# Performance work log

Hardware: AMD Instinct MI355X
Metric: run time of the kernel (lower is better)

The kernel has to match this reference:

```python
import jax, jax.numpy as jnp
import numpy as np

GRID_DIMS = (64, 64, 64)
GRID_LOWER = np.array([0.0, 0.0, 0.0], np.float32)
GRID_STEPS = np.array([0.015625, 0.015625, 0.015625], np.float32)
RADIUS = 0.03125
STENCIL = 2  # ceil(radius / step)


def _poly6(d2, h):
    # standard SPH poly6 smoothing kernel: 315/(64 pi h^9) (h^2 - d^2)^3, d <= h
    c = np.float32(315.0 / (64.0 * np.pi * h ** 9))
    return jnp.where(d2 <= h * h, c * (h * h - d2) ** 3, 0.0)


def particles2grid(locs, data, density):
    # locs [B,N,3], data [B,N,C], density [B,N] -> grid [B,X,Y,Z,C]
    B, N, _ = locs.shape
    C = data.shape[-1]
    X, Y, Z = GRID_DIMS
    dims = jnp.array(GRID_DIMS, jnp.int32)
    r = jnp.arange(-STENCIL, STENCIL + 1)
    offs = jnp.stack(jnp.meshgrid(r, r, r, indexing='ij'), -1).reshape(-1, 3)  # [K,3]
    base = jnp.floor((locs - GRID_LOWER) / GRID_STEPS).astype(jnp.int32)        # [B,N,3]
    cells = base[:, :, None, :] + offs                                          # [B,N,K,3]
    centers = GRID_LOWER + (cells.astype(locs.dtype) + 0.5) * GRID_STEPS
    d2 = jnp.sum((centers - locs[:, :, None, :]) ** 2, -1)                      # [B,N,K]
    w = _poly6(d2, RADIUS)
    w = jnp.where(jnp.all((cells >= 0) & (cells < dims), -1), w, 0.0)
    contrib = w[..., None] * (data / density[..., None])[:, :, None, :]         # [B,N,K,C]
    cells = jnp.clip(cells, 0, dims - 1)
    flat = (cells[..., 0] * Y + cells[..., 1]) * Z + cells[..., 2]              # [B,N,K]

    def splat(f, c):
        return jnp.zeros((X * Y * Z, C), data.dtype).at[f.reshape(-1)].add(c.reshape(-1, C))

    return jax.vmap(splat)(flat, contrib).reshape(B, X, Y, Z, C)


def grid2particles(grid, locs):
    # trilinear interpolation of grid [B,X,Y,Z,C] at particle locations [B,N,3]
    B, X, Y, Z, C = grid.shape
    dims = jnp.array([X, Y, Z], jnp.int32)
    pos = (locs - GRID_LOWER) / GRID_STEPS - 0.5                                # cell-center coords
    i0 = jnp.floor(pos).astype(jnp.int32)
    frac = pos - i0.astype(locs.dtype)
    gflat = grid.reshape(B, X * Y * Z, C)
    gather = jax.vmap(lambda g, f: g[f])                                        # [B,N] -> [B,N,C]
    out = jnp.zeros((B, locs.shape[1], C), grid.dtype)
    for dx in (0, 1):
        for dy in (0, 1):
            for dz in (0, 1):
                off = jnp.array([dx, dy, dz], jnp.int32)
                idx = i0 + off
                wd = jnp.where(off == 1, frac, 1.0 - frac)                      # [B,N,3]
                w = wd[..., 0] * wd[..., 1] * wd[..., 2]
                w = jnp.where(jnp.all((idx >= 0) & (idx < dims), -1), w, 0.0)
                idx = jnp.clip(idx, 0, dims - 1)
                flat = (idx[..., 0] * Y + idx[..., 1]) * Z + idx[..., 2]
                out = out + w[..., None] * gather(gflat, flat)
    return out


def conv3d(x, w, b):
    y = jax.lax.conv_general_dilated(x, w, (1, 1, 1), 'SAME',
                                     dimension_numbers=('NCDHW', 'OIDHW', 'NCDHW'))
    return y + b[None, :, None, None, None]


def prelu(x, a):
    return jnp.where(x >= 0, x, a * x)


def setup_inputs() -> dict:
    key = jax.random.key(0)
    ks = jax.random.split(key, 8)
    B, N = 2, 32768
    Cin, K, Cout = 4, 32, 4
    s = lambda fan: np.float32(1.0 / np.sqrt(fan * 27))
    return {
        'locs': jax.random.uniform(ks[0], (B, N, 3), jnp.float32),
        'data': jax.random.normal(ks[1], (B, N, Cin), jnp.float32),
        'density': jax.random.uniform(ks[2], (B, N), jnp.float32, 0.5, 1.5),
        'W0': jax.random.normal(ks[3], (K, Cin, 3, 3, 3), jnp.float32) * s(Cin),
        'b0': jnp.zeros((K,), jnp.float32),
        'W1': jax.random.normal(ks[4], (K, K, 3, 3, 3), jnp.float32) * s(K),
        'b1': jnp.zeros((K,), jnp.float32),
        'W2': jax.random.normal(ks[5], (K, K, 3, 3, 3), jnp.float32) * s(K),
        'b2': jnp.zeros((K,), jnp.float32),
        'W3': jax.random.normal(ks[6], (Cout, K, 3, 3, 3), jnp.float32) * s(K),
        'b3': jnp.zeros((Cout,), jnp.float32),
        'a0': jnp.full((1,), 0.25, jnp.float32),
        'a1': jnp.full((1,), 0.25, jnp.float32),
        'a2': jnp.full((1,), 0.25, jnp.float32),
    }


def reference(locs, data, density, W0, b0, W1, b1, W2, b2, W3, b3, a0, a1, a2):
    grid = particles2grid(locs, data, density)            # [B,X,Y,Z,Cin]
    g = jnp.transpose(grid, (0, 4, 1, 2, 3))              # NCDHW
    g = prelu(conv3d(g, W0, b0), a0)
    g = prelu(conv3d(g, W1, b1), a1)
    g = prelu(conv3d(g, W2, b2), a2)
    g = conv3d(g, W3, b3)
    g = jnp.transpose(g, (0, 2, 3, 4, 1))                 # [B,X,Y,Z,Cout]
    return grid2particles(g, locs)                        # [B,N,Cout]
```

## Files before the change

### kernel.cpp

```cpp
#include <hip/hip_runtime.h>

#define BATCH 2
#define NPART 32768
#define GD 64
#define NVOX (BATCH * GD * GD * GD)

typedef unsigned short ushortT;
typedef __attribute__((ext_vector_type(8))) short short8;
typedef __attribute__((ext_vector_type(16))) float float16;

__device__ __forceinline__ float poly6_c() {
    const double H9 = 1.0 / 35184372088832.0;
    return (float)(315.0 / (64.0 * 3.14159265358979323846 * H9));
}

__device__ __forceinline__ ushortT bf16_rne(float f) {
    unsigned int u = __float_as_uint(f);
    u = (u + 0x7fffu + ((u >> 16) & 1u)) >> 16;
    return (ushortT)u;
}

__device__ __forceinline__ int imax(int a, int b) { return a > b ? a : b; }
__device__ __forceinline__ int imin(int a, int b) { return a < b ? a : b; }

__device__ __forceinline__ void load_lds16(const void* g, void* l) {
    __builtin_amdgcn_global_load_lds(
        (const __attribute__((address_space(1))) void*)g,
        (__attribute__((address_space(3))) void*)l, 16, 0, 0);
}

__global__ __launch_bounds__(256) void prep_kernel(
    int* __restrict__ zp,
    const float* __restrict__ W0, const float* __restrict__ W1,
    const float* __restrict__ W2, const float* __restrict__ W3,
    short* __restrict__ Bp) {
    int bid = blockIdx.x, tid = threadIdx.x;
    if (bid < 513) {
        int t = bid * 256 + tid;
        if (t < 131088) zp[t] = 0;
        return;
    }
    int t = (bid - 513) * 256 + tid;
    if (t >= 176 * 512) return;
    int kt = t >> 9;
    int l = (t >> 3) & 63, j = t & 7;
    int n = l & 31, q = l >> 5;
    float v = 0.f;
    if (kt < 14) {
        int k = kt * 16 + 8 * q + j;
        int tap = k >> 3, ic = k & 7;
        if (tap < 27 && ic < 4) v = W0[(n * 4 + ic) * 27 + tap];
    } else {
        const float* W; int O, s;
        if (kt < 68)       { W = W1; O = 32; s = kt - 14; }
        else if (kt < 122) { W = W2; O = 32; s = kt - 68; }
        else               { W = W3; O = 4;  s = kt - 122; }
        int h = s / 27, ss = s - h * 27;
        int gI = ss / 3, dy = ss - gI * 3;
        int dx = gI / 3, dz = gI - dx * 3;
        int tap = dx * 9 + dy * 3 + dz;
        int ic = h * 16 + q * 8 + j;
        if (n < O) v = W[(n * 32 + ic) * 27 + tap];
    }
    Bp[t] = (short)bf16_rne(v);
}

__global__ __launch_bounds__(256) void bin_count_kernel(
    const float* __restrict__ locs, int* __restrict__ counts) {
    int t = blockIdx.x * blockDim.x + threadIdx.x;
    if (t >= BATCH * NPART) return;
    int b = t >> 15;
    int bx = ((int)floorf(locs[t * 3 + 0] * 64.0f)) >> 1;
    int by = ((int)floorf(locs[t * 3 + 1] * 64.0f)) >> 1;
    int bz = ((int)floorf(locs[t * 3 + 2] * 64.0f)) >> 1;
    atomicAdd(&counts[b * 32768 + ((bx * 32) + by) * 32 + bz], 1);
}

__global__ __launch_bounds__(256) void scanA_kernel(
    const int* __restrict__ counts, int* __restrict__ offsets,
    int* __restrict__ blockSum) {
    __shared__ int sh[256];
    int tid = threadIdx.x, g = blockIdx.x;
    int v = counts[g * 256 + tid];
    sh[tid] = v;
    __syncthreads();
    for (int off = 1; off < 256; off <<= 1) {
        int u = (tid >= off) ? sh[tid - off] : 0;
        __syncthreads();
        sh[tid] += u;
        __syncthreads();
    }
    offsets[g * 256 + tid] = sh[tid] - v;
    if (tid == 255) blockSum[g] = sh[255];
}

__global__ __launch_bounds__(256) void scanB_kernel(
    int* __restrict__ offsets, const int* __restrict__ blockSum) {
    __shared__ int sh[256];
    int tid = threadIdx.x, g = blockIdx.x;
    sh[tid] = (tid < g) ? blockSum[tid] : 0;
    __syncthreads();
    for (int off = 128; off > 0; off >>= 1) {
        if (tid < off) sh[tid] += sh[tid + off];
        __syncthreads();
    }
    offsets[g * 256 + tid] += sh[0];
    if (g == 255 && tid == 255) offsets[65536] = BATCH * NPART;
}

__global__ __launch_bounds__(256) void bin_scatter_kernel(
    const float* __restrict__ locs, const float* __restrict__ data,
    const float* __restrict__ density, const int* __restrict__ offsets,
    int* __restrict__ cursor, float* __restrict__ payload) {
    int t = blockIdx.x * blockDim.x + threadIdx.x;
    if (t >= BATCH * NPART) return;
    int b = t >> 15;
    float px = locs[t * 3 + 0];
    float py = locs[t * 3 + 1];
    float pz = locs[t * 3 + 2];
    int bx = ((int)floorf(px * 64.0f)) >> 1;
    int by = ((int)floorf(py * 64.0f)) >> 1;
    int bz = ((int)floorf(pz * 64.0f)) >> 1;
    int bb = b * 32768 + ((bx * 32) + by) * 32 + bz;
    int slot = atomicAdd(&cursor[bb], 1);
    int idx = offsets[bb] + slot;
    float inv_d = 1.0f / density[t];
    float4 p0 = {px, py, pz, data[t * 4 + 0] * inv_d};
    float4 p1 = {data[t * 4 + 1] * inv_d, data[t * 4 + 2] * inv_d,
                 data[t * 4 + 3] * inv_d, 0.f};
    *(float4*)(payload + idx * 8)     = p0;
    *(float4*)(payload + idx * 8 + 4) = p1;
}

__global__ __launch_bounds__(256) void splat_gather_kernel(
    const float* __restrict__ payload, const int* __restrict__ offsets,
    ushortT* __restrict__ g8) {
    __shared__ float plist[256 * 8];
    __shared__ int segS[36];
    __shared__ int segP[37];
    __shared__ int shTot[1];

    int wg = blockIdx.x;
    int sb = wg & 511, b = wg >> 9;
    int X0 = (sb >> 6) * 8, Y0 = ((sb >> 3) & 7) * 8, Z0 = (sb & 7) * 8;
    int tid = threadIdx.x;

    int bxlo = imax(0, (X0 - 2) >> 1), bxhi = imin(31, (X0 + 9) >> 1);
    int bylo = imax(0, (Y0 - 2) >> 1), byhi = imin(31, (Y0 + 9) >> 1);
    int bzlo = imax(0, (Z0 - 2) >> 1), bzhi = imin(31, (Z0 + 9) >> 1);
    int ny = byhi - bylo + 1;
    int ns = (bxhi - bxlo + 1) * ny;
    if (tid < ns) {
        int bx = bxlo + tid / ny, by = bylo + tid % ny;
        int row = b * 32768 + (bx * 32 + by) * 32;
        int s = offsets[row + bzlo];
        int e = offsets[row + bzhi + 1];
        segS[tid] = s;
        segP[tid] = e - s;
    }
    __syncthreads();
    if (tid == 0) {
        int p = 0;
        for (int k = 0; k < ns; ++k) { int len = segP[k]; segP[k] = p; p += len; }
        segP[ns] = p;
        shTot[0] = p;
    }
    __syncthreads();

    const float step = 0.015625f;
    const float h2 = 0.03125f * 0.03125f;
    const float cc = poly6_c();
    int total = shTot[0];

    int l = tid & 63, w = tid >> 6;
    int cx = X0 + 4 * (w >> 1) + (l >> 4);
    int cy = Y0 + 4 * (w & 1) + ((l >> 2) & 3);
    int cz0 = Z0 + (l & 3);
    float xc  = ((float)cx  + 0.5f) * step;
    float yc  = ((float)cy  + 0.5f) * step;
    float zc0 = ((float)cz0 + 0.5f) * step;
    float zc1 = zc0 + 4.0f * step;

    float a00 = 0.f, a01 = 0.f, a02 = 0.f, a03 = 0.f;
    float a10 = 0.f, a11 = 0.f, a12 = 0.f, a13 = 0.f;

    int nchunks = (total + 255) >> 8;
    for (int ch = 0; ch < nchunks; ++ch) {
        __syncthreads();
        int jj = (ch << 8) + tid;
        if (jj < total) {
            int k = 0;
            while (jj >= segP[k + 1]) ++k;
            int idx = segS[k] + (jj - segP[k]);
            *(float4*)(plist + tid * 8)     = *(const float4*)(payload + idx * 8);
            *(float4*)(plist + tid * 8 + 4) = *(const float4*)(payload + idx * 8 + 4);
        }
        __syncthreads();
        int cnt = imin(256, total - (ch << 8));
        for (int p = 0; p < cnt; ++p) {
            float4 pa = *(const float4*)(plist + p * 8);
            float dx = pa.x - xc, dy = pa.y - yc;
            float dxy2 = fmaf(dy, dy, dx * dx);
            if (!__any(dxy2 <= h2)) continue;
            float4 pv = *(const float4*)(plist + p * 8 + 4);
            float dz0 = pa.z - zc0;
            float d20 = fmaf(dz0, dz0, dxy2);
            float u0 = fmaxf(h2 - d20, 0.f);
            float w0 = (cc * u0) * (u0 * u0);
            a00 = fmaf(w0, pa.w, a00);
            a01 = fmaf(w0, pv.x, a01);
            a02 = fmaf(w0, pv.y, a02);
            a03 = fmaf(w0, pv.z, a03);
            float dz1 = pa.z - zc1;
            float d21 = fmaf(dz1, dz1, dxy2);
            float u1 = fmaxf(h2 - d21, 0.f);
            float w1 = (cc * u1) * (u1 * u1);
            a10 = fmaf(w1, pa.w, a10);
            a11 = fmaf(w1, pv.x, a11);
            a12 = fmaf(w1, pv.y, a12);
            a13 = fmaf(w1, pv.z, a13);
        }
    }

    size_t cellBase = (size_t)(((b * 64 + cx) * 64 + cy) * 64);
    short8 o;
    o[0] = (short)bf16_rne(a00); o[1] = (short)bf16_rne(a01);
    o[2] = (short)bf16_rne(a02); o[3] = (short)bf16_rne(a03);
    o[4] = 0; o[5] = 0; o[6] = 0; o[7] = 0;
    *(short8*)(g8 + (cellBase + cz0) * 8) = o;
    o[0] = (short)bf16_rne(a10); o[1] = (short)bf16_rne(a11);
    o[2] = (short)bf16_rne(a12); o[3] = (short)bf16_rne(a13);
    *(short8*)(g8 + (cellBase + cz0 + 4) * 8) = o;
}

template <int ICG, int KT, bool FINAL>
__global__ __launch_bounds__(256, 4) void mfma_conv_kernel(
    const ushortT* __restrict__ in, const short* __restrict__ Bpack,
    const float* __restrict__ bias, const float* __restrict__ alpha,
    const float* __restrict__ zguard, void* __restrict__ outv) {
    constexpr int CIN = ICG * 8;
    constexpr int NCH = (ICG == 1) ? (36 * 34) : (36 * 2 * 34);
    __shared__ short lds[NCH * 8];
    int wg = ((blockIdx.x & 7) << 7) | (blockIdx.x >> 3);
    int zh = wg & 1, yq = (wg >> 1) & 15, xp = (wg >> 5) & 15, b = wg >> 9;
    int X0 = xp * 4, Y0 = yq * 4, Z0 = zh * 32;
    int tid = threadIdx.x;

    const ushortT* inb = in + (size_t)b * (64 * 64 * 64 * CIN);

    int l = tid & 63, w = tid >> 6;
    int n = l & 31, q = l >> 5;

    float bval = FINAL ? (n < 4 ? bias[n] : 0.f) : bias[n];
    float16 acc0, acc1, acc2, acc3;
#pragma unroll
    for (int r = 0; r < 16; ++r) {
        acc0[r] = bval; acc1[r] = bval; acc2[r] = bval; acc3[r] = bval;
    }

    const short* bp = Bpack + (size_t)l * 8;
    int laneZ = (l & 31) * 8;

    short8 bf[4];
#pragma unroll
    for (int i = 0; i < 4; ++i) bf[i] = *(const short8*)(bp + i * 512);

    if constexpr (ICG == 1) {
#pragma unroll
        for (int it = 0; it < (NCH + 255) / 256; ++it) {
            int ccid = it * 256 + tid;
            if (ccid < NCH) {
                int col = ccid / 34;
                int zi  = ccid - col * 34;
                int gx = X0 + col / 6 - 1;
                int gy = Y0 + col % 6 - 1;
                int gz = Z0 + zi - 1;
                const void* src = (const void*)zguard;
                if ((unsigned)gx < 64u && (unsigned)gy < 64u && (unsigned)gz < 64u)
                    src = (const void*)(inb + ((size_t)(((gx * 64) + gy) * 64 + gz)) * CIN);
                load_lds16(src, (void*)(lds + ccid * 8));
            }
        }
        __syncthreads();
#pragma unroll
        for (int kt = 0; kt < KT; ++kt) {
            short8 bcur = bf[kt & 3];
            if (kt + 4 < KT) bf[kt & 3] = *(const short8*)(bp + (kt + 4) * 512);
            int tap0 = kt * 2, tap1 = kt * 2 + 1;
            if (tap1 > 26) tap1 = 26;
            int dx0 = tap0 / 9, r0 = tap0 - dx0 * 9, dy0 = r0 / 3, dz0 = r0 - dy0 * 3;
            int dx1 = tap1 / 9, r1 = tap1 - dx1 * 9, dy1 = r1 / 3, dz1 = r1 - dy1 * 3;
#define AOFS1(c) (q ? ((((w + dx1) * 6 + ((c) + dy1)) * 34 + dz1) * 8) \
                    : ((((w + dx0) * 6 + ((c) + dy0)) * 34 + dz0) * 8))
            short8 a0 = *(const short8*)(lds + AOFS1(0) + laneZ);
            short8 a1 = *(const short8*)(lds + AOFS1(1) + laneZ);
            short8 a2 = *(const short8*)(lds + AOFS1(2) + laneZ);
            short8 a3 = *(const short8*)(lds + AOFS1(3) + laneZ);
#undef AOFS1
            __builtin_amdgcn_s_setprio(1);
            acc0 = __builtin_amdgcn_mfma_f32_32x32x16_bf16(a0, bcur, acc0, 0, 0, 0);
            acc1 = __builtin_amdgcn_mfma_f32_32x32x16_bf16(a1, bcur, acc1, 0, 0, 0);
            acc2 = __builtin_amdgcn_mfma_f32_32x32x16_bf16(a2, bcur, acc2, 0, 0, 0);
            acc3 = __builtin_amdgcn_mfma_f32_32x32x16_bf16(a3, bcur, acc3, 0, 0, 0);
            __builtin_amdgcn_s_setprio(0);
        }
    } else {
#pragma unroll
        for (int h = 0; h < 2; ++h) {
            if (h) __syncthreads();
#pragma unroll
            for (int it = 0; it < (NCH + 255) / 256; ++it) {
                int ccid = it * 256 + tid;
                if (ccid < NCH) {
                    int col = ccid / 68;
                    int rem = ccid - col * 68;
                    int icg2 = rem / 34;
                    int zi   = rem - icg2 * 34;
                    int gx = X0 + col / 6 - 1;
                    int gy = Y0 + col % 6 - 1;
                    int gz = Z0 + zi - 1;
                    const void* src = (const void*)zguard;
                    if ((unsigned)gx < 64u && (unsigned)gy < 64u && (unsigned)gz < 64u)
                        src = (const void*)(inb +
                            ((size_t)(((gx * 64) + gy) * 64 + gz)) * CIN + (h * 2 + icg2) * 8);
                    load_lds16(src, (void*)(lds + ccid * 8));
                }
            }
            __syncthreads();
#pragma unroll
            for (int g = 0; g < 9; ++g) {
                int dx = g / 3, dz = g - dx * 3;
                short8 fr[6];
#pragma unroll
                for (int col = 0; col < 6; ++col) {
                    int ofs = ((((w + dx) * 6 + col) * 2 + q) * 34 + dz) * 8;
                    fr[col] = *(const short8*)(lds + ofs + laneZ);
                }
#pragma unroll
                for (int dy = 0; dy < 3; ++dy) {
                    int kt = h * 27 + g * 3 + dy;
                    short8 bcur = bf[kt & 3];
                    if (kt + 4 < KT) bf[kt & 3] = *(const short8*)(bp + (kt + 4) * 512);
                    __builtin_amdgcn_s_setprio(1);
                    acc0 = __builtin_amdgcn_mfma_f32_32x32x16_bf16(fr[0 + dy], bcur, acc0, 0, 0, 0);
                    acc1 = __builtin_amdgcn_mfma_f32_32x32x16_bf16(fr[1 + dy], bcur, acc1, 0, 0, 0);
                    acc2 = __builtin_amdgcn_mfma_f32_32x32x16_bf16(fr[2 + dy], bcur, acc2, 0, 0, 0);
                    acc3 = __builtin_amdgcn_mfma_f32_32x32x16_bf16(fr[3 + dy], bcur, acc3, 0, 0, 0);
                    __builtin_amdgcn_s_setprio(0);
                }
            }
        }
    }

    size_t base0 = (size_t)(((b * 64 + X0 + w) * 64 + Y0) * 64) + Z0;
    if (FINAL) {
        float* out = (float*)outv;
        if (n < 4) {
#pragma unroll
            for (int r = 0; r < 16; ++r) {
                int z = (r & 3) + 8 * (r >> 2) + 4 * q;
                out[(base0 + z) * 4 + n]        = acc0[r];
                out[(base0 + 64 + z) * 4 + n]   = acc1[r];
                out[(base0 + 128 + z) * 4 + n]  = acc2[r];
                out[(base0 + 192 + z) * 4 + n]  = acc3[r];
            }
        }
    } else {
        float a = alpha[0];
        ushortT* out = (ushortT*)outv;
#pragma unroll
        for (int r = 0; r < 16; ++r) {
            int z = (r & 3) + 8 * (r >> 2) + 4 * q;
            float v0 = acc0[r]; v0 = v0 >= 0.f ? v0 : a * v0;
            out[(base0 + z) * 32 + n] = bf16_rne(v0);
            float v1 = acc1[r]; v1 = v1 >= 0.f ? v1 : a * v1;
            out[(base0 + 64 + z) * 32 + n] = bf16_rne(v1);
            float v2 = acc2[r]; v2 = v2 >= 0.f ? v2 : a * v2;
            out[(base0 + 128 + z) * 32 + n] = bf16_rne(v2);
            float v3 = acc3[r]; v3 = v3 >= 0.f ? v3 : a * v3;
            out[(base0 + 192 + z) * 32 + n] = bf16_rne(v3);
        }
    }
}

__global__ __launch_bounds__(256) void gather_kernel(
    const float* __restrict__ grid, const float* __restrict__ locs,
    float* __restrict__ out) {
    int t = blockIdx.x * blockDim.x + threadIdx.x;
    if (t >= BATCH * NPART) return;
    int b = t >> 15;

    float px = locs[t * 3 + 0] * 64.0f - 0.5f;
    float py = locs[t * 3 + 1] * 64.0f - 0.5f;
    float pz = locs[t * 3 + 2] * 64.0f - 0.5f;
    int ix = (int)floorf(px);
    int iy = (int)floorf(py);
    int iz = (int)floorf(pz);
    float fx = px - (float)ix;
    float fy = py - (float)iy;
    float fz = pz - (float)iz;

    const float* gb = grid + (size_t)b * GD * GD * GD * 4;
    float o0 = 0.f, o1 = 0.f, o2 = 0.f, o3 = 0.f;

#pragma unroll
    for (int dx = 0; dx < 2; ++dx) {
        int x = ix + dx;
        if ((unsigned)x > 63u) continue;
        float wx = dx ? fx : 1.0f - fx;
#pragma unroll
        for (int dy = 0; dy < 2; ++dy) {
            int y = iy + dy;
            if ((unsigned)y > 63u) continue;
            float wy = dy ? fy : 1.0f - fy;
#pragma unroll
            for (int dz = 0; dz < 2; ++dz) {
                int z = iz + dz;
                if ((unsigned)z > 63u) continue;
                float wz = dz ? fz : 1.0f - fz;
                float w = wx * wy * wz;
                const float4 g = *(const float4*)(gb + (size_t)(((x * GD) + y) * GD + z) * 4);
                o0 += w * g.x; o1 += w * g.y; o2 += w * g.z; o3 += w * g.w;
            }
        }
    }
    out[t * 4 + 0] = o0;
    out[t * 4 + 1] = o1;
    out[t * 4 + 2] = o2;
    out[t * 4 + 3] = o3;
}

extern "C" void kernel_launch(void* const* d_in, const int* in_sizes, int n_in,
                              void* d_out, int out_size, void* d_ws, size_t ws_size,
                              hipStream_t stream) {
    const float* locs    = (const float*)d_in[0];
    const float* data    = (const float*)d_in[1];
    const float* density = (const float*)d_in[2];
    const float* W0 = (const float*)d_in[3];
    const float* b0 = (const float*)d_in[4];
    const float* W1 = (const float*)d_in[5];
    const float* b1 = (const float*)d_in[6];
    const float* W2 = (const float*)d_in[7];
    const float* b2 = (const float*)d_in[8];
    const float* W3 = (const float*)d_in[9];
    const float* b3 = (const float*)d_in[10];
    const float* a0 = (const float*)d_in[11];
    const float* a1 = (const float*)d_in[12];
    const float* a2 = (const float*)d_in[13];
    float* out = (float*)d_out;

    char* ws = (char*)d_ws;
    ushortT* g8  = (ushortT*)(ws);
    ushortT* gA  = (ushortT*)(ws + 8388608);
    ushortT* gB  = (ushortT*)(ws + 41943040);
    float*  gF   = (float*)(ws + 75497472);
    short*  Bp   = (short*)(ws + 83886080);
    short*  Bp0  = Bp;
    short*  Bp1  = Bp + 14 * 512;
    short*  Bp2  = Bp + 68 * 512;
    short*  Bp3  = Bp + 122 * 512;
    float* zguard   = (float*)(ws + 84066240);
    int*   counts   = (int*)(ws + 84066304);
    int*   cursor   = (int*)(ws + 84328448);
    int*   offsets  = (int*)(ws + 84590592);
    int*   blockSum = (int*)(ws + 84852752);
    float* payload  = (float*)(ws + 84853888);

    prep_kernel<<<513 + 352, 256, 0, stream>>>((int*)zguard, W0, W1, W2, W3, Bp);

    bin_count_kernel<<<(BATCH * NPART) / 256, 256, 0, stream>>>(locs, counts);
    scanA_kernel<<<256, 256, 0, stream>>>(counts, offsets, blockSum);
    scanB_kernel<<<256, 256, 0, stream>>>(offsets, blockSum);
    bin_scatter_kernel<<<(BATCH * NPART) / 256, 256, 0, stream>>>(
        locs, data, density, offsets, cursor, payload);

    splat_gather_kernel<<<BATCH * 512, 256, 0, stream>>>(payload, offsets, g8);

    const int CGRID = 1024;
    mfma_conv_kernel< 1, 14, false><<<CGRID, 256, 0, stream>>>(g8, Bp0, b0, a0, zguard, gA);
    mfma_conv_kernel< 4, 54, false><<<CGRID, 256, 0, stream>>>(gA, Bp1, b1, a1, zguard, gB);
    mfma_conv_kernel< 4, 54, false><<<CGRID, 256, 0, stream>>>(gB, Bp2, b2, a2, zguard, gA);
    mfma_conv_kernel< 4, 54, true ><<<CGRID, 256, 0, stream>>>(gA, Bp3, b3, b3, zguard, gF);

    gather_kernel<<<(BATCH * NPART) / 256, 256, 0, stream>>>(gF, locs, out);
}
```

Measured before the change: 269.2 us.

## Double-buffer LDS staging in conv kernel, each block processes both z-halves

The 3D conv kernel now has each workgroup handle both 32-deep z tiles, with two LDS buffers so the async global-to-LDS load of the next phase (channel half or z tile) overlaps with MFMA compute on the current one. The grid is halved to 512 blocks and launch bounds drop to 2 blocks per CU because LDS use doubles. The goal is to hide input staging latency behind matrix work, at the cost of fewer resident waves and less parallelism across the 256 CUs.

```diff
diff --git a/kernel.cpp b/kernel.cpp
--- a/kernel.cpp
+++ b/kernel.cpp
@@ -234,151 +234,159 @@
 }
 
 template <int ICG, int KT, bool FINAL>
-__global__ __launch_bounds__(256, 4) void mfma_conv_kernel(
+__global__ __launch_bounds__(256, 2) void mfma_conv_kernel(
     const ushortT* __restrict__ in, const short* __restrict__ Bpack,
     const float* __restrict__ bias, const float* __restrict__ alpha,
     const float* __restrict__ zguard, void* __restrict__ outv) {
-    constexpr int CIN = ICG * 8;
-    constexpr int NCH = (ICG == 1) ? (36 * 34) : (36 * 2 * 34);
-    __shared__ short lds[NCH * 8];
-    int wg = ((blockIdx.x & 7) << 7) | (blockIdx.x >> 3);
-    int zh = wg & 1, yq = (wg >> 1) & 15, xp = (wg >> 5) & 15, b = wg >> 9;
-    int X0 = xp * 4, Y0 = yq * 4, Z0 = zh * 32;
+    constexpr int CIN  = ICG * 8;
+    constexpr int PH   = (ICG == 1) ? 1 : 2;
+    constexpr int NCHP = (ICG == 1) ? (36 * 34) : (36 * 2 * 34);
+    constexpr int BUFS = NCHP * 8;
+    __shared__ short lds[2 * BUFS];
+
+    int wg2 = ((blockIdx.x & 7) << 6) | (blockIdx.x >> 3);
+    int yq = wg2 & 15, xp = (wg2 >> 4) & 15, b = wg2 >> 8;
+    int X0 = xp * 4, Y0 = yq * 4;
     int tid = threadIdx.x;
-
     const ushortT* inb = in + (size_t)b * (64 * 64 * 64 * CIN);
 
     int l = tid & 63, w = tid >> 6;
     int n = l & 31, q = l >> 5;
-
+    int laneZ = (l & 31) * 8;
+    const short* bp = Bpack + (size_t)l * 8;
     float bval = FINAL ? (n < 4 ? bias[n] : 0.f) : bias[n];
-    float16 acc0, acc1, acc2, acc3;
-#pragma unroll
-    for (int r = 0; r < 16; ++r) {
-        acc0[r] = bval; acc1[r] = bval; acc2[r] = bval; acc3[r] = bval;
-    }
-
-    const short* bp = Bpack + (size_t)l * 8;
-    int laneZ = (l & 31) * 8;
-
-    short8 bf[4];
-#pragma unroll
-    for (int i = 0; i < 4; ++i) bf[i] = *(const short8*)(bp + i * 512);
-
-    if constexpr (ICG == 1) {
-#pragma unroll
-        for (int it = 0; it < (NCH + 255) / 256; ++it) {
+
+    auto stage = [&](int ph) {
+        int t = ph / PH, h = ph - t * PH;
+        int zb = t * 32;
+        short* dst = lds + (ph & 1) * BUFS;
+#pragma unroll
+        for (int it = 0; it < (NCHP + 255) / 256; ++it) {
             int ccid = it * 256 + tid;
-            if (ccid < NCH) {
-                int col = ccid / 34;
-                int zi  = ccid - col * 34;
+            if (ccid < NCHP) {
+                int col, icg2, zi;
+                if constexpr (ICG == 1) {
+                    col = ccid / 34; zi = ccid - col * 34; icg2 = 0;
+                } else {
+                    col = ccid / 68;
+                    int rem = ccid - col * 68;
+                    icg2 = rem / 34; zi = rem - icg2 * 34;
+                }
                 int gx = X0 + col / 6 - 1;
                 int gy = Y0 + col % 6 - 1;
-                int gz = Z0 + zi - 1;
+                int gz = zb + zi - 1;
                 const void* src = (const void*)zguard;
                 if ((unsigned)gx < 64u && (unsigned)gy < 64u && (unsigned)gz < 64u)
-                    src = (const void*)(inb + ((size_t)(((gx * 64) + gy) * 64 + gz)) * CIN);
-                load_lds16(src, (void*)(lds + ccid * 8));
+                    src = (const void*)(inb +
+                        ((size_t)(((gx * 64) + gy) * 64 + gz)) * CIN + (h * 2 + icg2) * 8);
+                load_lds16(src, (void*)(dst + ccid * 8));
             }
         }
-        __syncthreads();
-#pragma unroll
-        for (int kt = 0; kt < KT; ++kt) {
-            short8 bcur = bf[kt & 3];
-            if (kt + 4 < KT) bf[kt & 3] = *(const short8*)(bp + (kt + 4) * 512);
-            int tap0 = kt * 2, tap1 = kt * 2 + 1;
-            if (tap1 > 26) tap1 = 26;
-            int dx0 = tap0 / 9, r0 = tap0 - dx0 * 9, dy0 = r0 / 3, dz0 = r0 - dy0 * 3;
-            int dx1 = tap1 / 9, r1 = tap1 - dx1 * 9, dy1 = r1 / 3, dz1 = r1 - dy1 * 3;
+    };
+
+    stage(0);
+
+#pragma unroll
+    for (int tile = 0; tile < 2; ++tile) {
+        int Z0 = tile * 32;
+        float16 acc0, acc1, acc2, acc3;
+#pragma unroll
+        for (int r = 0; r < 16; ++r) {
+            acc0[r] = bval; acc1[r] = bval; acc2[r] = bval; acc3[r] = bval;
+        }
+
+#pragma unroll
+        for (int h = 0; h < PH; ++h) {
+            int ph = tile * PH + h;
+            __syncthreads();
+            if (ph + 1 < 2 * PH) stage(ph + 1);
+            const short* lb = lds + (ph & 1) * BUFS;
+
+            if constexpr (ICG == 1) {
+                short8 bf[4];
+#pragma unroll
+                for (int i = 0; i < 4; ++i) bf[i] = *(const short8*)(bp + i * 512);
+#pragma unroll
+                for (int kt = 0; kt < KT; ++kt) {
+                    short8 bcur = bf[kt & 3];
+                    if (kt + 4 < KT) bf[kt & 3] = *(const short8*)(bp + (kt + 4) * 512);
+                    int tap0 = kt * 2, tap1 = kt * 2 + 1;
+                    if (tap1 > 26) tap1 = 26;
+                    int dx0 = tap0 / 9, r0 = tap0 - dx0 * 9, dy0 = r0 / 3, dz0 = r0 - dy0 * 3;
+                    int dx1 = tap1 / 9, r1 = tap1 - dx1 * 9, dy1 = r1 / 3, dz1 = r1 - dy1 * 3;
 #define AOFS1(c) (q ? ((((w + dx1) * 6 + ((c) + dy1)) * 34 + dz1) * 8) \
                     : ((((w + dx0) * 6 + ((c) + dy0)) * 34 + dz0) * 8))
-            short8 a0 = *(const short8*)(lds + AOFS1(0) + laneZ);
-            short8 a1 = *(const short8*)(lds + AOFS1(1) + laneZ);
-            short8 a2 = *(const short8*)(lds + AOFS1(2) + laneZ);
-            short8 a3 = *(const short8*)(lds + AOFS1(3) + laneZ);
+                    short8 a0 = *(const short8*)(lb + AOFS1(0) + laneZ);
+                    short8 a1 = *(const short8*)(lb + AOFS1(1) + laneZ);
+                    short8 a2 = *(const short8*)(lb + AOFS1(2) + laneZ);
+                    short8 a3 = *(const short8*)(lb + AOFS1(3) + laneZ);
 #undef AOFS1
-            __builtin_amdgcn_s_setprio(1);
-            acc0 = __builtin_amdgcn_mfma_f32_32x32x16_bf16(a0, bcur, acc0, 0, 0, 0);
-            acc1 = __builtin_amdgcn_mfma_f32_32x32x16_bf16(a1, bcur, acc1, 0, 0, 0);
-            acc2 = __builtin_amdgcn_mfma_f32_32x32x16_bf16(a2, bcur, acc2, 0, 0, 0);
-            acc3 = __builtin_amdgcn_mfma_f32_32x32x16_bf16(a3, bcur, acc3, 0, 0, 0);
-            __builtin_amdgcn_s_setprio(0);
-        }
-    } else {
-#pragma unroll
-        for (int h = 0; h < 2; ++h) {
-            if (h) __syncthreads();
-#pragma unroll
-            for (int it = 0; it < (NCH + 255) / 256; ++it) {
-                int ccid = it * 256 + tid;
-                if (ccid < NCH) {
-                    int col = ccid / 68;
-                    int rem = ccid - col * 68;
-                    int icg2 = rem / 34;
-                    int zi   = rem - icg2 * 34;
-                    int gx = X0 + col / 6 - 1;
-                    int gy = Y0 + col % 6 - 1;
-                    int gz = Z0 + zi - 1;
-                    const void* src = (const void*)zguard;
-                    if ((unsigned)gx < 64u && (unsigned)gy < 64u && (unsigned)gz < 64u)
-                        src = (const void*)(inb +
-                            ((size_t)(((gx * 64) + gy) * 64 + gz)) * CIN + (h * 2 + icg2) * 8);
-                    load_lds16(src, (void*)(lds + ccid * 8));
+                    __builtin_amdgcn_s_setprio(1);
+                    acc0 = __builtin_amdgcn_mfma_f32_32x32x16_bf16(a0, bcur, acc0, 0, 0, 0);
+                    acc1 = __builtin_amdgcn_mfma_f32_32x32x16_bf16(a1, bcur, acc1, 0, 0, 0);
+                    acc2 = __builtin_amdgcn_mfma_f32_32x32x16_bf16(a2, bcur, acc2, 0, 0, 0);
+                    acc3 = __builtin_amdgcn_mfma_f32_32x32x16_bf16(a3, bcur, acc3, 0, 0, 0);
+                    __builtin_amdgcn_s_setprio(0);
+                }
+            } else {
+                short8 bf[4];
+#pragma unroll
+                for (int i = 0; i < 4; ++i)
+                    bf[i] = *(const short8*)(bp + (h * 27 + i) * 512);
+#pragma unroll
+                for (int g = 0; g < 9; ++g) {
+                    int dx = g / 3, dz = g - dx * 3;
+                    short8 fr[6];
+#pragma unroll
+                    for (int col = 0; col < 6; ++col) {
+                        int ofs = ((((w + dx) * 6 + col) * 2 + q) * 34 + dz) * 8;
+                        fr[col] = *(const short8*)(lb + ofs + laneZ);
+                    }
+#pragma unroll
+                    for (int dy = 0; dy < 3; ++dy) {
+                        int k27 = g * 3 + dy;
+                        short8 bcur = bf[k27 & 3];
+                        if (k27 + 4 < 27)
+                            bf[k27 & 3] = *(const short8*)(bp + (h * 27 + k27 + 4) * 512);
+                        __builtin_amdgcn_s_setprio(1);
+                        acc0 = __builtin_amdgcn_mfma_f32_32x32x16_bf16(fr[0 + dy], bcur, acc0, 0, 0, 0);
+                        acc1 = __builtin_amdgcn_mfma_f32_32x32x16_bf16(fr[1 + dy], bcur, acc1, 0, 0, 0);
+                        acc2 = __builtin_amdgcn_mfma_f32_32x32x16_bf16(fr[2 + dy], bcur, acc2, 0, 0, 0);
+                        acc3 = __builtin_amdgcn_mfma_f32_32x32x16_bf16(fr[3 + dy], bcur, acc3, 0, 0, 0);
+                        __builtin_amdgcn_s_setprio(0);
+                    }
                 }
             }
-            __syncthreads();
-#pragma unroll
-            for (int g = 0; g < 9; ++g) {
-                int dx = g / 3, dz = g - dx * 3;
-                short8 fr[6];
-#pragma unroll
-                for (int col = 0; col < 6; ++col) {
-                    int ofs = ((((w + dx) * 6 + col) * 2 + q) * 34 + dz) * 8;
-                    fr[col] = *(const short8*)(lds + ofs + laneZ);
-                }
-#pragma unroll
-                for (int dy = 0; dy < 3; ++dy) {
-                    int kt = h * 27 + g * 3 + dy;
-                    short8 bcur = bf[kt & 3];
-                    if (kt + 4 < KT) bf[kt & 3] = *(const short8*)(bp + (kt + 4) * 512);
-                    __builtin_amdgcn_s_setprio(1);
-                    acc0 = __builtin_amdgcn_mfma_f32_32x32x16_bf16(fr[0 + dy], bcur, acc0, 0, 0, 0);
-                    acc1 = __builtin_amdgcn_mfma_f32_32x32x16_bf16(fr[1 + dy], bcur, acc1, 0, 0, 0);
-                    acc2 = __builtin_amdgcn_mfma_f32_32x32x16_bf16(fr[2 + dy], bcur, acc2, 0, 0, 0);
-                    acc3 = __builtin_amdgcn_mfma_f32_32x32x16_bf16(fr[3 + dy], bcur, acc3, 0, 0, 0);
-                    __builtin_amdgcn_s_setprio(0);
+        }
+
+        size_t base0 = (size_t)(((b * 64 + X0 + w) * 64 + Y0) * 64) + Z0;
+        if constexpr (FINAL) {
+            float* out = (float*)outv;
+            if (n < 4) {
+#pragma unroll
+                for (int r = 0; r < 16; ++r) {
+                    int z = (r & 3) + 8 * (r >> 2) + 4 * q;
+                    out[(base0 + z) * 4 + n]        = acc0[r];
+                    out[(base0 + 64 + z) * 4 + n]   = acc1[r];
+                    out[(base0 + 128 + z) * 4 + n]  = acc2[r];
+                    out[(base0 + 192 + z) * 4 + n]  = acc3[r];
                 }
             }
-        }
-    }
-
-    size_t base0 = (size_t)(((b * 64 + X0 + w) * 64 + Y0) * 64) + Z0;
-    if (FINAL) {
-        float* out = (float*)outv;
-        if (n < 4) {
+        } else {
+            float a = alpha[0];
+            ushortT* out = (ushortT*)outv;
 #pragma unroll
             for (int r = 0; r < 16; ++r) {
                 int z = (r & 3) + 8 * (r >> 2) + 4 * q;
-                out[(base0 + z) * 4 + n]        = acc0[r];
-                out[(base0 + 64 + z) * 4 + n]   = acc1[r];
-                out[(base0 + 128 + z) * 4 + n]  = acc2[r];
-                out[(base0 + 192 + z) * 4 + n]  = acc3[r];
+                float v0 = acc0[r]; v0 = v0 >= 0.f ? v0 : a * v0;
+                out[(base0 + z) * 32 + n] = bf16_rne(v0);
+                float v1 = acc1[r]; v1 = v1 >= 0.f ? v1 : a * v1;
+                out[(base0 + 64 + z) * 32 + n] = bf16_rne(v1);
+                float v2 = acc2[r]; v2 = v2 >= 0.f ? v2 : a * v2;
+                out[(base0 + 128 + z) * 32 + n] = bf16_rne(v2);
+                float v3 = acc3[r]; v3 = v3 >= 0.f ? v3 : a * v3;
+                out[(base0 + 192 + z) * 32 + n] = bf16_rne(v3);
             }
-        }
-    } else {
-        float a = alpha[0];
-        ushortT* out = (ushortT*)outv;
-#pragma unroll
-        for (int r = 0; r < 16; ++r) {
-            int z = (r & 3) + 8 * (r >> 2) + 4 * q;
-            float v0 = acc0[r]; v0 = v0 >= 0.f ? v0 : a * v0;
-            out[(base0 + z) * 32 + n] = bf16_rne(v0);
-            float v1 = acc1[r]; v1 = v1 >= 0.f ? v1 : a * v1;
-            out[(base0 + 64 + z) * 32 + n] = bf16_rne(v1);
-            float v2 = acc2[r]; v2 = v2 >= 0.f ? v2 : a * v2;
-            out[(base0 + 128 + z) * 32 + n] = bf16_rne(v2);
-            float v3 = acc3[r]; v3 = v3 >= 0.f ? v3 : a * v3;
-            out[(base0 + 192 + z) * 32 + n] = bf16_rne(v3);
         }
     }
 }
@@ -476,7 +484,7 @@
 
     splat_gather_kernel<<<BATCH * 512, 256, 0, stream>>>(payload, offsets, g8);
 
-    const int CGRID = 1024;
+    const int CGRID = 512;
     mfma_conv_kernel< 1, 14, false><<<CGRID, 256, 0, stream>>>(g8, Bp0, b0, a0, zguard, gA);
     mfma_conv_kernel< 4, 54, false><<<CGRID, 256, 0, stream>>>(gA, Bp1, b1, a1, zguard, gB);
     mfma_conv_kernel< 4, 54, false><<<CGRID, 256, 0, stream>>>(gB, Bp2, b2, a2, zguard, gA);
```

New measurement: 242.9 us. 1.11x faster.
